# Kernel optimization log

Measured on AMD Instinct MI355X. Metric: run time of the kernel, lower is better.

The kernel has to match this reference:

```python
import jax, jax.numpy as jnp
import numpy as np

SCALE = 64.0   # CosFace scale s
MARGIN = 0.35  # CosFace margin m
EPS = 1e-12


def setup_inputs() -> dict:
    key = jax.random.key(0)
    k1, k2, k3 = jax.random.split(key, 3)
    batch, feat_dim, num_classes = 512, 512, 100000
    return {
        "input": jax.random.normal(k1, (batch, feat_dim), dtype=jnp.float32),
        "label": jax.random.randint(k2, (batch,), 0, num_classes, dtype=jnp.int64),
        "w": jax.random.normal(k3, (feat_dim, num_classes), dtype=jnp.float32),
    }


def reference(input, label, w):
    # L2-normalize features (rows) and class weights (columns), as in _forward_train
    feat_norm = jnp.clip(jnp.linalg.norm(input, axis=1, keepdims=True), EPS, None)
    normed_feat = input / feat_norm                      # [B, D]
    w_norm = jnp.clip(jnp.linalg.norm(w, axis=0, keepdims=True), EPS, None)
    normed_w = w / w_norm                                # [D, C]
    cosine = jnp.clip(normed_feat @ normed_w, -1.0, 1.0)  # [B, C]
    # CosFace margin applied at the true-label position (get_probs_i)
    onehot = jax.nn.one_hot(label, w.shape[1], dtype=cosine.dtype)
    logits = SCALE * (cosine - MARGIN * onehot)          # [B, C]
    # loss = mean(logsumexp over all (sharded) classes - logit at true label)
    lse = jax.nn.logsumexp(logits, axis=1)               # [B]
    x = jnp.take_along_axis(logits, label[:, None], axis=1)[:, 0]  # [B]
    return jnp.mean(lse - x)
```

## Files before the change

### kernel.cpp

```cpp
#include <hip/hip_runtime.h>
#include <hip/hip_bf16.h>
#include <math.h>

#define BDIM 512
#define DDIM 512
#define CDIM 100000
#define NC 64
#define BM 128
#define BN 128
#define BK 64
#define NKSTEP (DDIM / BK)
#define GNB 782
#define CPADT 100096
#define NCHT (CPADT / NC)
#define NBLK (GNB * 4)
#define CTILE 128

typedef __attribute__((ext_vector_type(8))) short short8;
typedef __attribute__((ext_vector_type(4))) float f32x4;

__device__ __forceinline__ unsigned short f2bf(float f) {
  unsigned int u = __builtin_bit_cast(unsigned int, f);
  u = (u + 0x7FFFu + ((u >> 16) & 1u)) >> 16;
  return (unsigned short)u;
}

__device__ __forceinline__ void gl_lds16(const unsigned short* g, unsigned short* l) {
  __builtin_amdgcn_global_load_lds(
      (const __attribute__((address_space(1))) void*)g,
      (__attribute__((address_space(3))) void*)l, 16, 0, 0);
}

__global__ void k_rownorm(const float* __restrict__ x, unsigned short* __restrict__ a) {
  const int b = blockIdx.x;
  const int tid = threadIdx.x;
  const float* row = x + (size_t)b * DDIM;
  float v0 = row[tid], v1 = row[tid + 256];
  float ss = v0 * v0 + v1 * v1;
  #pragma unroll
  for (int m = 1; m < 64; m <<= 1) ss += __shfl_xor(ss, m);
  __shared__ float sred[4];
  __shared__ float sinv;
  if ((tid & 63) == 0) sred[tid >> 6] = ss;
  __syncthreads();
  if (tid == 0) {
    float s = sred[0] + sred[1] + sred[2] + sred[3];
    sinv = 1.f / fmaxf(sqrtf(s), 1e-12f);
  }
  __syncthreads();
  const float inv = sinv;
  a[(size_t)b * DDIM + tid] = f2bf(v0 * inv);
  a[(size_t)b * DDIM + tid + 256] = f2bf(v1 * inv);
}

__global__ __launch_bounds__(512)
void k_wt(const float* __restrict__ w, unsigned short* __restrict__ wt,
          float* __restrict__ invwn) {
  __shared__ float tile[64][CTILE + 4];
  const int t = threadIdx.x;
  const int c0w = blockIdx.x * CTILE;
  const int rd_d = t >> 3;
  const int rd_c = (t & 7) * 16;
  const int wc = t >> 2;
  const int wh = t & 3;
  float ss = 0.f;

  for (int ch = 0; ch < 8; ch++) {
    const int d0 = ch * 64;
    float4 r[4];
    #pragma unroll
    for (int j = 0; j < 4; j++) {
      const int c = c0w + rd_c + j * 4;
      if (c + 3 < CDIM)
        r[j] = *reinterpret_cast<const float4*>(w + (size_t)(d0 + rd_d) * CDIM + c);
      else {
        #pragma unroll
        for (int e = 0; e < 4; e++)
          r[j][e] = (c + e < CDIM) ? w[(size_t)(d0 + rd_d) * CDIM + c + e] : 0.f;
      }
    }
    #pragma unroll
    for (int j = 0; j < 4; j++)
      *reinterpret_cast<float4*>(&tile[rd_d][rd_c + j * 4]) = r[j];
    __syncthreads();

    short8 o0, o1;
    #pragma unroll
    for (int j = 0; j < 8; j++) {
      const float v = tile[wh * 16 + j][wc];
      ss += v * v;
      o0[j] = (short)f2bf(v);
    }
    #pragma unroll
    for (int j = 0; j < 8; j++) {
      const float v = tile[wh * 16 + 8 + j][wc];
      ss += v * v;
      o1[j] = (short)f2bf(v);
    }
    {
      unsigned short* dst = wt + ((size_t)(c0w + wc) << 9) + d0 + wh * 16;
      *reinterpret_cast<short8*>(dst) = o0;
      *reinterpret_cast<short8*>(dst + 8) = o1;
    }
    __syncthreads();
  }
  ss += __shfl_xor(ss, 1);
  ss += __shfl_xor(ss, 2);
  if (wh == 0)
    invwn[c0w + wc] = (c0w + wc < CDIM) ? 1.f / fmaxf(sqrtf(ss), 1e-12f) : 1.f;
}

__global__ __launch_bounds__(256, 4)
void k_main(const unsigned short* __restrict__ a,
            const unsigned short* __restrict__ wt,
            const float* __restrict__ invwn,
            const long long* __restrict__ label,
            float2* __restrict__ part,
            float* __restrict__ labellogit) {
  __shared__ __align__(16) unsigned short alds[BM * BK];
  __shared__ __align__(16) unsigned short blds[BN * BK];

  const int t = threadIdx.x;
  const int orig = (blockIdx.x & 7) * (NBLK / 8) + (blockIdx.x >> 3);
  const int rb = orig & 3;
  const int cb = orig >> 2;
  const int bm0 = rb * BM;
  const int bn0 = cb * BN;

  const int wave = t >> 6;
  const int lane = t & 63;
  const int wr = wave >> 1;
  const int wc = wave & 1;
  const int lhi = lane >> 4;
  const int llo = lane & 15;
  const int l8 = lane & 7;

  auto stage = [&](int s) {
    #pragma unroll
    for (int i = 0; i < 4; i++) {
      const int row = wave * 32 + i * 8 + (lane >> 3);
      const int piece = l8 ^ (lane >> 3);
      gl_lds16(a + (size_t)(bm0 + row) * DDIM + s * BK + piece * 8,
               &alds[(wave * 32 + i * 8) * BK]);
      gl_lds16(wt + ((size_t)(bn0 + row) << 9) + s * BK + piece * 8,
               &blds[(wave * 32 + i * 8) * BK]);
    }
  };

  f32x4 acc[4][4];
  #pragma unroll
  for (int i = 0; i < 4; i++)
    #pragma unroll
    for (int j = 0; j < 4; j++)
      acc[i][j] = (f32x4){0.f, 0.f, 0.f, 0.f};

  #pragma unroll
  for (int s = 0; s < NKSTEP; s++) {
    stage(s);
    __syncthreads();

    #pragma unroll
    for (int kk = 0; kk < 2; kk++) {
      short8 af[4], bfr[4];
      #pragma unroll
      for (int m = 0; m < 4; m++) {
        const int row = wr * 64 + m * 16 + llo;
        const int pc = (kk * 4 + lhi) ^ (row & 7);
        af[m] = *reinterpret_cast<const short8*>(&alds[row * BK + pc * 8]);
      }
      #pragma unroll
      for (int n = 0; n < 4; n++) {
        const int col = wc * 64 + n * 16 + llo;
        const int pc = (kk * 4 + lhi) ^ (col & 7);
        bfr[n] = *reinterpret_cast<const short8*>(&blds[col * BK + pc * 8]);
      }
      #pragma unroll
      for (int m = 0; m < 4; m++)
        #pragma unroll
        for (int n = 0; n < 4; n++)
          acc[m][n] = __builtin_amdgcn_mfma_f32_16x16x32_bf16(af[m], bfr[n], acc[m][n], 0, 0, 0);
    }

    __syncthreads();
  }

  float inv[4];
  #pragma unroll
  for (int n = 0; n < 4; n++)
    inv[n] = invwn[bn0 + wc * 64 + n * 16 + llo];

  const int chunk = cb * 2 + wc;
  #pragma unroll
  for (int m = 0; m < 4; m++) {
    #pragma unroll
    for (int r = 0; r < 4; r++) {
      const int row = bm0 + wr * 64 + m * 16 + (lhi << 2) + r;
      const int lab = (int)label[row];
      float vals[4];
      float mloc = -100.0f;
      #pragma unroll
      for (int n = 0; n < 4; n++) {
        const int cg = bn0 + wc * 64 + n * 16 + llo;
        float cs = acc[m][n][r] * inv[n];
        cs = fminf(fmaxf(cs, -1.f), 1.f);
        float lg = 64.f * cs;
        if (cg == lab) { lg = 64.f * (cs - 0.35f); labellogit[row] = lg; }
        if (cg >= CDIM) lg = -INFINITY;
        vals[n] = lg;
        mloc = fmaxf(mloc, lg);
      }
      float mm = mloc;
      #pragma unroll
      for (int msk = 1; msk < 16; msk <<= 1) mm = fmaxf(mm, __shfl_xor(mm, msk));
      float sacc = 0.f;
      #pragma unroll
      for (int n = 0; n < 4; n++) sacc += __expf(vals[n] - mm);
      #pragma unroll
      for (int msk = 1; msk < 16; msk <<= 1) sacc += __shfl_xor(sacc, msk);
      if (llo == 0) part[(size_t)chunk * BDIM + row] = make_float2(mm, sacc);
    }
  }
}

__global__ void k_rowreduce(const float2* __restrict__ part,
                            const float* __restrict__ labellogit,
                            float* __restrict__ rowloss) {
  const int row = blockIdx.x;
  const int tid = threadIdx.x;
  float m = -INFINITY, s = 0.f;
  for (int ch = tid; ch < NCHT; ch += 256) {
    float2 p = part[(size_t)ch * BDIM + row];
    float nm = fmaxf(m, p.x);
    s = s * __expf(m - nm) + p.y * __expf(p.x - nm);
    m = nm;
  }
  #pragma unroll
  for (int msk = 1; msk < 64; msk <<= 1) {
    float om = __shfl_xor(m, msk), os = __shfl_xor(s, msk);
    float nm = fmaxf(m, om);
    s = s * __expf(m - nm) + os * __expf(om - nm);
    m = nm;
  }
  __shared__ float sm[4], ssum[4];
  const int wv = tid >> 6, ln = tid & 63;
  if (ln == 0) { sm[wv] = m; ssum[wv] = s; }
  __syncthreads();
  if (tid == 0) {
    float M = sm[0], S = ssum[0];
    #pragma unroll
    for (int i = 1; i < 4; i++) {
      float nm = fmaxf(M, sm[i]);
      S = S * __expf(M - nm) + ssum[i] * __expf(sm[i] - nm);
      M = nm;
    }
    rowloss[row] = M + logf(S) - labellogit[row];
  }
}

__global__ void k_mean(const float* __restrict__ rowloss, float* __restrict__ out) {
  const int tid = threadIdx.x;
  float v = rowloss[tid];
  #pragma unroll
  for (int msk = 1; msk < 64; msk <<= 1) v += __shfl_xor(v, msk);
  __shared__ float sred[8];
  if ((tid & 63) == 0) sred[tid >> 6] = v;
  __syncthreads();
  if (tid == 0) {
    float s = 0.f;
    #pragma unroll
    for (int i = 0; i < 8; i++) s += sred[i];
    out[0] = s / (float)BDIM;
  }
}

extern "C" void kernel_launch(void* const* d_in, const int* in_sizes, int n_in,
                              void* d_out, int out_size, void* d_ws, size_t ws_size,
                              hipStream_t stream) {
  const float* input = (const float*)d_in[0];
  const long long* label = (const long long*)d_in[1];
  const float* w = (const float*)d_in[2];
  float* out = (float*)d_out;

  char* ws = (char*)d_ws;
  unsigned short* a_bf16 = (unsigned short*)(ws + 0);
  float2* part           = (float2*)(ws + 524288);
  float* labellogit      = (float*)(ws + 6930432);
  float* rowloss         = (float*)(ws + 6932480);
  float* invwn           = (float*)(ws + 6934528);
  unsigned short* w_t    = (unsigned short*)(ws + 7334912);

  k_rownorm<<<BDIM, 256, 0, stream>>>(input, a_bf16);
  k_wt<<<CPADT / CTILE, 512, 0, stream>>>(w, w_t, invwn);
  k_main<<<NBLK, 256, 0, stream>>>(a_bf16, w_t, invwn, label, part, labellogit);
  k_rowreduce<<<BDIM, 256, 0, stream>>>(part, labellogit, rowloss);
  k_mean<<<1, BDIM, 0, stream>>>(rowloss, out);
}
```

Baseline: 176.2 us.

## Double-buffer LDS tiles with BK=32 to overlap global loads with MFMA

Halves the K tile to 32 and allocates two LDS buffers for A and B, prefetching step s+1 via global_load_lds while computing step s. This removes one barrier per K step and is meant to hide global-to-LDS latency behind the MFMA work. The swizzle is reworked for the 64-byte row stride. The trade-off is twice as many K iterations, with less MFMA work per sync, and the same LDS footprint. There is also a risk that the async LDS loads are not properly waited on before the barrier.

Measured after the change: 181.6 us. 3.1% more time.

```diff
diff --git a/kernel.cpp b/kernel.cpp
--- a/kernel.cpp
+++ b/kernel.cpp
@@ -8,7 +8,7 @@
 #define NC 64
 #define BM 128
 #define BN 128
-#define BK 64
+#define BK 32
 #define NKSTEP (DDIM / BK)
 #define GNB 782
 #define CPADT 100096
@@ -117,8 +117,8 @@
             const long long* __restrict__ label,
             float2* __restrict__ part,
             float* __restrict__ labellogit) {
-  __shared__ __align__(16) unsigned short alds[BM * BK];
-  __shared__ __align__(16) unsigned short blds[BN * BK];
+  __shared__ __align__(16) unsigned short alds[2][BM * BK];
+  __shared__ __align__(16) unsigned short blds[2][BN * BK];
 
   const int t = threadIdx.x;
   const int orig = (blockIdx.x & 7) * (NBLK / 8) + (blockIdx.x >> 3);
@@ -133,17 +133,16 @@
   const int wc = wave & 1;
   const int lhi = lane >> 4;
   const int llo = lane & 15;
-  const int l8 = lane & 7;
-
-  auto stage = [&](int s) {
-    #pragma unroll
-    for (int i = 0; i < 4; i++) {
-      const int row = wave * 32 + i * 8 + (lane >> 3);
-      const int piece = l8 ^ (lane >> 3);
-      gl_lds16(a + (size_t)(bm0 + row) * DDIM + s * BK + piece * 8,
-               &alds[(wave * 32 + i * 8) * BK]);
-      gl_lds16(wt + ((size_t)(bn0 + row) << 9) + s * BK + piece * 8,
-               &blds[(wave * 32 + i * 8) * BK]);
+
+  auto stage = [&](int s, int buf) {
+    #pragma unroll
+    for (int i = 0; i < 2; i++) {
+      const int r = wave * 32 + i * 16 + (lane >> 2);
+      const int piece = (lane & 3) ^ ((r >> 1) & 3);
+      gl_lds16(a + (size_t)(bm0 + r) * DDIM + s * BK + piece * 8,
+               &alds[buf][(wave * 32 + i * 16) * BK]);
+      gl_lds16(wt + ((size_t)(bn0 + r) << 9) + s * BK + piece * 8,
+               &blds[buf][(wave * 32 + i * 16) * BK]);
     }
   };
 
@@ -154,32 +153,32 @@
     for (int j = 0; j < 4; j++)
       acc[i][j] = (f32x4){0.f, 0.f, 0.f, 0.f};
 
+  stage(0, 0);
+  __syncthreads();
+
   #pragma unroll
   for (int s = 0; s < NKSTEP; s++) {
-    stage(s);
-    __syncthreads();
-
-    #pragma unroll
-    for (int kk = 0; kk < 2; kk++) {
-      short8 af[4], bfr[4];
-      #pragma unroll
-      for (int m = 0; m < 4; m++) {
-        const int row = wr * 64 + m * 16 + llo;
-        const int pc = (kk * 4 + lhi) ^ (row & 7);
-        af[m] = *reinterpret_cast<const short8*>(&alds[row * BK + pc * 8]);
-      }
-      #pragma unroll
-      for (int n = 0; n < 4; n++) {
-        const int col = wc * 64 + n * 16 + llo;
-        const int pc = (kk * 4 + lhi) ^ (col & 7);
-        bfr[n] = *reinterpret_cast<const short8*>(&blds[col * BK + pc * 8]);
-      }
-      #pragma unroll
-      for (int m = 0; m < 4; m++)
-        #pragma unroll
-        for (int n = 0; n < 4; n++)
-          acc[m][n] = __builtin_amdgcn_mfma_f32_16x16x32_bf16(af[m], bfr[n], acc[m][n], 0, 0, 0);
-    }
+    if (s + 1 < NKSTEP) stage(s + 1, (s + 1) & 1);
+
+    const int buf = s & 1;
+    short8 af[4], bfr[4];
+    #pragma unroll
+    for (int m = 0; m < 4; m++) {
+      const int row = wr * 64 + m * 16 + llo;
+      const int pc = lhi ^ ((row >> 1) & 3);
+      af[m] = *reinterpret_cast<const short8*>(&alds[buf][row * BK + pc * 8]);
+    }
+    #pragma unroll
+    for (int n = 0; n < 4; n++) {
+      const int col = wc * 64 + n * 16 + llo;
+      const int pc = lhi ^ ((col >> 1) & 3);
+      bfr[n] = *reinterpret_cast<const short8*>(&blds[buf][col * BK + pc * 8]);
+    }
+    #pragma unroll
+    for (int m = 0; m < 4; m++)
+      #pragma unroll
+      for (int n = 0; n < 4; n++)
+        acc[m][n] = __builtin_amdgcn_mfma_f32_16x16x32_bf16(af[m], bfr[n], acc[m][n], 0, 0, 0);
 
     __syncthreads();
   }
```
